# Optimization experiments

Measured on AMD Instinct MI355X. Metric: run time of the kernel, lower is better.

Reference implementation:

```python
import jax, jax.numpy as jnp
import numpy as np

ALPHABET = 8
DIM = 128
SEQ_LEN = 8192
POWER_ITERS = 200


def setup_inputs() -> dict:
    key = jax.random.key(0)
    k1, k2, k3 = jax.random.split(key, 3)
    return {
        "Kraus_op_re": jax.random.uniform(k1, (ALPHABET, DIM, DIM), dtype=jnp.float32),
        "Kraus_op_im": jax.random.uniform(k2, (ALPHABET, DIM, DIM), dtype=jnp.float32),
        "sequence": jax.random.randint(k3, (SEQ_LEN,), 0, ALPHABET),
    }


def _leading_eig(K):
    # K: [A, d, d] complex. Power iteration on the transfer map and its adjoint.
    d = K.shape[-1]
    Kc = K.conj()

    def body_r(rhor, _):
        # rhov = sum_x K_x @ rhor @ K_x^H
        rhov = jnp.einsum("aij,jk,alk->il", K, rhor, Kc)
        mu = jnp.trace(rhov).real
        return rhov / mu.astype(rhov.dtype), None

    rhor, _ = jax.lax.scan(body_r, jnp.eye(d, dtype=K.dtype) / d, None, length=POWER_ITERS)

    def body_l(carry, _):
        rhol, _ = carry
        # rhov = sum_x K_x^H @ rhol @ K_x
        rhov = jnp.einsum("aji,jk,akl->il", Kc, rhol, K)
        mu = jnp.trace(rhov).real
        return (rhov / mu.astype(rhov.dtype), mu), None

    (rhol, mu), _ = jax.lax.scan(
        body_l, (jnp.eye(d, dtype=K.dtype), jnp.asarray(1.0, jnp.float32)), None, length=POWER_ITERS
    )
    return rhor, rhol, mu


def reference(Kraus_op_re, Kraus_op_im, sequence):
    K = Kraus_op_re.astype(jnp.complex64) + 1j * Kraus_op_im.astype(jnp.complex64)
    rhor, rhol, lam = _leading_eig(K)
    # normalize so that trace(rho @ rhol) == 1
    rho0 = rhor / jnp.trace(rhor @ rhol).real.astype(rhor.dtype)
    Kn = K / jnp.sqrt(lam).astype(K.dtype)  # Kraus ops rescaled by sqrt(leading eigenvalue)
    L = sequence.shape[0]

    def step(carry, inp):
        rho, logp = carry
        i, x = inp
        Kx = Kn[x]
        rho = Kx @ rho @ Kx.conj().T
        px = jnp.where(i == L - 1, jnp.trace(rho @ rhol).real, jnp.trace(rho).real)
        logp = logp - jnp.log2(px)
        rho = rho / px.astype(rho.dtype)
        return (rho, logp), None

    (_, log_p), _ = jax.lax.scan(
        step, (rho0, jnp.asarray(0.0, jnp.float32)), (jnp.arange(L), sequence)
    )
    return log_p[None]  # matches torch.tensor([0.0]) accumulator shape (1,)
```

## Files before the change

kernel.cpp:

```cpp
#include <hip/hip_runtime.h>

typedef unsigned int u32;
typedef unsigned short u16;
typedef __attribute__((ext_vector_type(4))) float f32x4;
typedef __attribute__((ext_vector_type(8))) short s16x8;
typedef __attribute__((ext_vector_type(4))) u32 u32x4;

#define DIMN 128
#define MATN (DIMN*DIMN)
#define NA 8
#define LSEQ 8192
#define NTOK (LSEQ/2)
#define PITERS 4
#define S1SH 5
#define S2SH 6
#define CHSH 7
#define P2SH 8
#define GCH 256
#define GLG 16

struct WS {
  float2 *Kc;
  u16 *Kb, *P2b, *rho, *nodes0, *nodes1, *rootR, *rootI;
  int *tok, *E0, *E1, *Eroot;
  float *trbuf;
  float *out;
};

__device__ __forceinline__ u16 f2bf(float x){
  u32 u = __float_as_uint(x);
  u32 r = (u + 0x7FFFu + ((u >> 16) & 1u)) >> 16;
  return (u16)r;
}
__device__ __forceinline__ float bf2f(u16 u){ return __uint_as_float(((u32)u) << 16); }
__device__ __forceinline__ u32 cvtpk(float lo, float hi){
  u32 r; asm("v_cvt_pk_bf16_f32 %0, %1, %2" : "=v"(r) : "v"(lo), "v"(hi)); return r;
}
__device__ __forceinline__ s16x8 negi(s16x8 v){
  return __builtin_bit_cast(s16x8, __builtin_bit_cast(u32x4, v) ^ 0x80008000u);
}
__device__ __forceinline__ int swz16(int maj, int b){
  return maj*256 + (((((b >> 4) + maj*5) & 15) << 4) | (b & 15));
}
__device__ __forceinline__ void cfma2(float2& c, float2 a, float2 b){
  c.x = fmaf(a.x, b.x, c.x); c.x = fmaf(-a.y, b.y, c.x);
  c.y = fmaf(a.x, b.y, c.y); c.y = fmaf(a.y, b.x, c.y);
}
template<int CA, int CB>
__device__ __forceinline__ void cmfma(s16x8 a_r, s16x8 a_i, s16x8 b_r, s16x8 b_i,
                                      f32x4& qr, f32x4& qi){
  s16x8 t1 = (CA ^ CB) ? a_i : negi(a_i);
  s16x8 t2 = CB ? negi(a_r) : a_r;
  s16x8 t3 = CA ? negi(a_i) : a_i;
  qr = __builtin_amdgcn_mfma_f32_16x16x32_bf16(a_r, b_r, qr, 0,0,0);
  qr = __builtin_amdgcn_mfma_f32_16x16x32_bf16(t1,  b_i, qr, 0,0,0);
  qi = __builtin_amdgcn_mfma_f32_16x16x32_bf16(t2,  b_i, qi, 0,0,0);
  qi = __builtin_amdgcn_mfma_f32_16x16x32_bf16(t3,  b_r, qi, 0,0,0);
}

__global__ __launch_bounds__(256) void k_init(const float* Kre, const float* Kim,
                                              const int* seq, WS w){
  int gid = blockIdx.x*256 + threadIdx.x;
  int gsz = gridDim.x*256;
  for (int i = gid; i < NA*MATN; i += gsz){
    int x = i / MATN, rem = i - x*MATN, r = rem >> 7, c = rem & 127;
    float re = Kre[i], im = Kim[i];
    w.Kc[i] = make_float2(re, im);
    u16* b = w.Kb + (size_t)x*4*MATN;
    b[rem] = f2bf(re); b[MATN + rem] = f2bf(im);
    b[2*MATN + c*128 + r] = f2bf(re); b[3*MATN + c*128 + r] = f2bf(im);
  }
  for (int i = gid; i < NTOK; i += gsz)
    w.tok[i] = seq[2*i+1]*NA + seq[2*i];
  for (int i = gid; i < 4*MATN; i += gsz){
    int plane = (i >> 14) & 1, rem = i & (MATN-1);
    u16 v = (plane == 0 && (rem >> 7) == (rem & 127)) ? f2bf(1.f) : (u16)0;
    w.rho[i] = v;
  }
  if (gid < 32) w.trbuf[gid] = 0.f;
}

__global__ __launch_bounds__(256) void k_p2(WS w){
  __shared__ float2 As[16][33], Bs[16][33];
  int blk = blockIdx.x, mat = blk >> 4, tile = blk & 15;
  int a = mat >> 3, b = mat & 7;
  int row0 = (tile>>2)*32, col0 = (tile&3)*32;
  int t = threadIdx.x, ti = t & 15, tk = t >> 4;
  const float2* A = w.Kc + a*MATN;
  const float2* B = w.Kc + b*MATN;
  float2 acc[4] = {{0,0},{0,0},{0,0},{0,0}};
  for (int k0 = 0; k0 < 128; k0 += 16){
    { int r = t >> 4, kk = t & 15;
      As[kk][r]    = A[(row0+r)*DIMN + k0+kk];
      As[kk][r+16] = A[(row0+r+16)*DIMN + k0+kk]; }
    { int kk = t >> 5, c = t & 31;
      Bs[kk][c]   = B[(k0+kk)*DIMN + col0+c];
      Bs[kk+8][c] = B[(k0+kk+8)*DIMN + col0+c]; }
    __syncthreads();
    #pragma unroll
    for (int jj = 0; jj < 16; jj++){
      float2 a0 = As[jj][ti], a1 = As[jj][ti+16];
      float2 b0 = Bs[jj][tk], b1 = Bs[jj][tk+16];
      cfma2(acc[0], a0, b0); cfma2(acc[1], a0, b1);
      cfma2(acc[2], a1, b0); cfma2(acc[3], a1, b1);
    }
    __syncthreads();
  }
  const float sc = 1.f/(1<<P2SH);
  u16* base = w.P2b + (size_t)mat*4*MATN;
  int rr[4] = {row0+ti, row0+ti, row0+ti+16, row0+ti+16};
  int cc[4] = {col0+tk, col0+tk+16, col0+tk, col0+tk+16};
  #pragma unroll
  for (int i = 0; i < 4; i++){
    u16 vr = f2bf(acc[i].x*sc), vi = f2bf(acc[i].y*sc);
    base[rr[i]*128 + cc[i]] = vr;            base[MATN + rr[i]*128 + cc[i]] = vi;
    base[2*MATN + cc[i]*128 + rr[i]] = vr;   base[3*MATN + cc[i]*128 + rr[i]] = vi;
  }
}

__device__ __forceinline__ void loadA(const u16* Ar, const u16* Ai,
    int wr, int l15, int hi, s16x8 (&fr)[4][2], s16x8 (&fi)[4][2]){
  #pragma unroll
  for (int kk = 0; kk < 4; kk++){
    int kb = kk*32 + hi*8;
    #pragma unroll
    for (int m = 0; m < 2; m++){
      int r = wr + m*16 + l15;
      fr[kk][m] = *(const s16x8*)(Ar + r*128 + kb);
      fi[kk][m] = *(const s16x8*)(Ai + r*128 + kb);
    }
  }
}
__device__ __forceinline__ void ccomputeR(const s16x8 (&fr)[4][2], const s16x8 (&fi)[4][2],
    const char* Pr, const char* Pi, f32x4 (&qr)[2][4], f32x4 (&qi)[2][4],
    int wc, int l15, int hi){
  #pragma unroll
  for (int m=0;m<2;m++)
    #pragma unroll
    for (int n=0;n<4;n++){ qr[m][n] = (f32x4){0,0,0,0}; qi[m][n] = (f32x4){0,0,0,0}; }
  #pragma unroll
  for (int kk = 0; kk < 4; kk++){
    int kb = kk*32 + hi*8;
    #pragma unroll
    for (int n=0;n<4;n++){
      int c = wc + n*16 + l15;
      int o = swz16(c, kb*2);
      s16x8 b_r = *(const s16x8*)(Pr + o);
      s16x8 b_i = *(const s16x8*)(Pi + o);
      #pragma unroll
      for (int m=0;m<2;m++)
        cmfma<0,0>(fr[kk][m], fi[kk][m], b_r, b_i, qr[m][n], qi[m][n]);
    }
  }
}
__device__ __forceinline__ void pwrite8(char* Pr, char* Pi,
    f32x4 (&qr)[2][4], f32x4 (&qi)[2][4], float sc, int t){
  int wv = t>>6, lane = t&63, l15 = lane&15, hi = lane>>4;
  int wr = (wv>>1)*32, wc = (wv&1)*64;
  #pragma unroll
  for (int m=0;m<2;m++)
    #pragma unroll
    for (int n=0;n<4;n++){
      int c = wc + n*16 + l15, r0 = wr + m*16 + hi*4;
      uint2 pr, pi;
      pr.x = cvtpk(qr[m][n][0]*sc, qr[m][n][1]*sc);
      pr.y = cvtpk(qr[m][n][2]*sc, qr[m][n][3]*sc);
      pi.x = cvtpk(qi[m][n][0]*sc, qi[m][n][1]*sc);
      pi.y = cvtpk(qi[m][n][2]*sc, qi[m][n][3]*sc);
      int o = swz16(c, r0*2);
      *(uint2*)(Pr + o) = pr;
      *(uint2*)(Pi + o) = pi;
    }
}
__device__ __forceinline__ int renorm8(char* Pr, char* Pi,
    f32x4 (&qr)[2][4], f32x4 (&qi)[2][4], int t){
  int wv = t>>6, lane = t&63;
  float lm = 0.f;
  #pragma unroll
  for (int m=0;m<2;m++)
    #pragma unroll
    for (int n=0;n<4;n++)
      #pragma unroll
      for (int j=0;j<4;j++)
        lm = fmaxf(lm, fmaxf(fabsf(qr[m][n][j]), fabsf(qi[m][n][j])));
  #pragma unroll
  for (int o = 32; o > 0; o >>= 1) lm = fmaxf(lm, __shfl_xor(lm, o, 64));
  if (lane == 0) ((float*)Pr)[wv] = lm;
  __syncthreads();
  float mx = 0.f;
  #pragma unroll
  for (int i = 0; i < 8; i++) mx = fmaxf(mx, ((float*)Pr)[i]);
  int e = 0; if (mx > 0.f) frexpf(mx, &e);
  __syncthreads();
  pwrite8(Pr, Pi, qr, qi, ldexpf(1.f, -e), t);
  return e;
}
__device__ __forceinline__ void stage_cols(const u16* gr, const u16* gi,
                                           char* Pr, char* Pi, int t){
  #pragma unroll
  for (int i = 0; i < 4; i++){
    int chunk = t + i*512;
    int c = chunk >> 4, rr = chunk & 15;
    int o = swz16(c, rr*16);
    *(uint4*)(Pr + o) = *(const uint4*)(gr + c*128 + rr*8);
    *(uint4*)(Pi + o) = *(const uint4*)(gi + c*128 + rr*8);
  }
}
__device__ __forceinline__ void write_node(u16* dr, u16* di,
    const char* Pr, const char* Pi, bool rowLayout, int t){
  if (!rowLayout){
    #pragma unroll
    for (int i = 0; i < 4; i++){
      int chunk = t + i*512;
      int c = chunk >> 4, rr = chunk & 15;
      int o = swz16(c, rr*16);
      *(uint4*)(dr + c*128 + rr*8) = *(const uint4*)(Pr + o);
      *(uint4*)(di + c*128 + rr*8) = *(const uint4*)(Pi + o);
    }
  } else {
    for (int idx = t; idx < MATN; idx += 512){
      int r = idx >> 7, c = idx & 127;
      int o = swz16(c, r*2);
      dr[idx] = *(const u16*)(Pr + o);
      di[idx] = *(const u16*)(Pi + o);
    }
  }
}

__global__ __launch_bounds__(512,2) void k_chain(WS w){
  __shared__ __align__(16) char Pr[32768];
  __shared__ __align__(16) char Pi[32768];
  int p = blockIdx.x, t = threadIdx.x;
  int wv = t>>6, lane = t&63, l15 = lane&15, hi = lane>>4;
  int wr = (wv>>1)*32, wc = (wv&1)*64;
  int tok0 = w.tok[p*GLG];
  const u16* b0 = w.P2b + (size_t)tok0*4*MATN;
  stage_cols(b0 + 2*MATN, b0 + 3*MATN, Pr, Pi, t);
  s16x8 A1r[4][2], A1i[4][2], A2r[4][2], A2i[4][2];
  { const u16* tb = w.P2b + (size_t)w.tok[p*GLG + 1]*4*MATN;
    loadA(tb, tb + MATN, wr, l15, hi, A1r, A1i); }
  f32x4 qr[2][4], qi[2][4];
  int eLast = 0;
  __syncthreads();
  for (int s = 1; s < GLG; s += 2){
    if (s+1 < GLG){
      const u16* tb = w.P2b + (size_t)w.tok[p*GLG + s+1]*4*MATN;
      loadA(tb, tb + MATN, wr, l15, hi, A2r, A2i);
    }
    ccomputeR(A1r, A1i, Pr, Pi, qr, qi, wc, l15, hi);
    __syncthreads();
    if (s < GLG-1){ pwrite8(Pr, Pi, qr, qi, 1.f/(1<<CHSH), t); }
    else { eLast = renorm8(Pr, Pi, qr, qi, t); }
    __syncthreads();
    if (s+1 < GLG){
      if (s+2 < GLG){
        const u16* tb = w.P2b + (size_t)w.tok[p*GLG + s+2]*4*MATN;
        loadA(tb, tb + MATN, wr, l15, hi, A1r, A1i);
      }
      ccomputeR(A2r, A2i, Pr, Pi, qr, qi, wc, l15, hi);
      __syncthreads();
      if (s+1 < GLG-1){ pwrite8(Pr, Pi, qr, qi, 1.f/(1<<CHSH), t); }
      else { eLast = renorm8(Pr, Pi, qr, qi, t); }
      __syncthreads();
    }
  }
  u16* slot = w.nodes0 + (size_t)p*2*MATN;
  write_node(slot, slot + MATN, Pr, Pi, (p & 3) != 0, t);
  if (t == 0) w.E0[p] = P2SH*GLG + CHSH*(GLG-2) + eLast;
}

__global__ __launch_bounds__(512,2) void k_level(WS w, int lvl){
  __shared__ __align__(16) char Pr[32768];
  __shared__ __align__(16) char Pi[32768];
  int p = blockIdx.x, t = threadIdx.x;
  int wv = t>>6, lane = t&63, l15 = lane&15, hi = lane>>4;
  int wr = (wv>>1)*32, wc = (wv&1)*64;
  const u16* src = (lvl & 1) ? w.nodes0 : w.nodes1;
  u16* dst       = (lvl & 1) ? w.nodes1 : w.nodes0;
  const int* Es  = (lvl & 1) ? w.E0 : w.E1;
  int* Ed        = (lvl & 1) ? w.E1 : w.E0;
  const u16* B = src + (size_t)(4*p)*2*MATN;
  stage_cols(B, B + MATN, Pr, Pi, t);
  int E = Es[4*p] + Es[4*p+1] + Es[4*p+2] + Es[4*p+3];
  s16x8 A1r[4][2], A1i[4][2], A2r[4][2], A2i[4][2];
  { const u16* A = src + (size_t)(4*p+1)*2*MATN;
    loadA(A, A + MATN, wr, l15, hi, A1r, A1i); }
  f32x4 qr[2][4], qi[2][4];
  __syncthreads();
  { const u16* A = src + (size_t)(4*p+2)*2*MATN;
    loadA(A, A + MATN, wr, l15, hi, A2r, A2i); }
  ccomputeR(A1r, A1i, Pr, Pi, qr, qi, wc, l15, hi);
  __syncthreads();
  E += renorm8(Pr, Pi, qr, qi, t);
  __syncthreads();
  { const u16* A = src + (size_t)(4*p+3)*2*MATN;
    loadA(A, A + MATN, wr, l15, hi, A1r, A1i); }
  ccomputeR(A2r, A2i, Pr, Pi, qr, qi, wc, l15, hi);
  __syncthreads();
  E += renorm8(Pr, Pi, qr, qi, t);
  __syncthreads();
  ccomputeR(A1r, A1i, Pr, Pi, qr, qi, wc, l15, hi);
  __syncthreads();
  E += renorm8(Pr, Pi, qr, qi, t);
  __syncthreads();
  bool isRoot = (gridDim.x == 1);
  u16* slot = dst + (size_t)p*2*MATN;
  write_node(slot, slot + MATN, Pr, Pi, ((p & 3) != 0) || isRoot, t);
  if (t == 0) Ed[p] = E;
}

__global__ __launch_bounds__(512,1) void k_pow(WS w, int par){
  __shared__ __align__(16) char Rr[32768];
  __shared__ __align__(16) char Ri[32768];
  __shared__ __align__(16) char Yr[32768];
  __shared__ __align__(16) char Yi[32768];
  int b = blockIdx.x, side = b >> 3, rb = b & 7;
  int t = threadIdx.x, wv = t>>6, lane = t&63, l15 = lane&15, hi = lane>>4;
  const u16* rhoS = w.rho + (size_t)((par*2 + side)*2)*MATN;
  stage_cols(rhoS, rhoS + MATN, Rr, Ri, t);
  __syncthreads();
  {
    int x = wv;
    const u16* Ab = w.Kb + (size_t)(x*4 + (side ? 2 : 0))*MATN;
    const u16* Ar = Ab; const u16* Ai = Ab + MATN;
    f32x4 q1r[8], q1i[8];
    #pragma unroll
    for (int n=0;n<8;n++){ q1r[n] = (f32x4){0,0,0,0}; q1i[n] = (f32x4){0,0,0,0}; }
    #pragma unroll
    for (int kk = 0; kk < 4; kk++){
      int kb = kk*32 + hi*8;
      int r = rb*16 + l15;
      s16x8 a_r = *(const s16x8*)(Ar + r*128 + kb);
      s16x8 a_i = *(const s16x8*)(Ai + r*128 + kb);
      #pragma unroll
      for (int n=0;n<8;n++){
        int c = n*16 + l15;
        int o = swz16(c, kb*2);
        s16x8 b_r = *(const s16x8*)(Rr + o);
        s16x8 b_i = *(const s16x8*)(Ri + o);
        if (side == 0) cmfma<0,0>(a_r, a_i, b_r, b_i, q1r[n], q1i[n]);
        else           cmfma<1,0>(a_r, a_i, b_r, b_i, q1r[n], q1i[n]);
      }
    }
    const float sc = 1.f/(1<<S1SH);
    #pragma unroll
    for (int n=0;n<8;n++)
      #pragma unroll
      for (int q=0;q<4;q++){
        int lr = hi*4 + q, c = n*16 + l15;
        *(u16*)(Yr + x*4096 + swz16(lr, c*2)) = f2bf(q1r[n][q]*sc);
        *(u16*)(Yi + x*4096 + swz16(lr, c*2)) = f2bf(q1i[n][q]*sc);
      }
  }
  __syncthreads();
  {
    int c0 = wv*16, c = c0 + l15;
    f32x4 q2r = {0,0,0,0}, q2i = {0,0,0,0};
    #pragma unroll 2
    for (int x = 0; x < 8; x++){
      const u16* Bb = w.Kb + (size_t)(x*4 + (side ? 2 : 0))*MATN;
      const u16* Br = Bb; const u16* Bi = Bb + MATN;
      #pragma unroll
      for (int kk = 0; kk < 4; kk++){
        int kb = kk*32 + hi*8;
        s16x8 a_r = *(const s16x8*)(Yr + x*4096 + swz16(l15, kb*2));
        s16x8 a_i = *(const s16x8*)(Yi + x*4096 + swz16(l15, kb*2));
        s16x8 b_r = *(const s16x8*)(Br + c*128 + kb);
        s16x8 b_i = *(const s16x8*)(Bi + c*128 + kb);
        if (side == 0) cmfma<0,1>(a_r, a_i, b_r, b_i, q2r, q2i);
        else           cmfma<0,0>(a_r, a_i, b_r, b_i, q2r, q2i);
      }
    }
    const float sc = 1.f/(1<<S2SH);
    u16* Dr = w.rho + (size_t)(((par^1)*2 + side)*2)*MATN;
    u16* Di = Dr + MATN;
    int r0g = rb*16 + hi*4;
    uint2 pr, pi;
    pr.x = cvtpk(q2r[0]*sc, q2r[1]*sc); pr.y = cvtpk(q2r[2]*sc, q2r[3]*sc);
    pi.x = cvtpk(q2i[0]*sc, q2i[1]*sc); pi.y = cvtpk(q2i[2]*sc, q2i[3]*sc);
    *(uint2*)(Dr + c*128 + r0g) = pr;
    *(uint2*)(Di + c*128 + r0g) = pi;
    if (side == 1 && wv == rb){
      float tr = 0.f;
      #pragma unroll
      for (int q=0;q<4;q++) if (hi*4 + q == l15) tr += q2r[q]*sc;
      #pragma unroll
      for (int o = 32; o > 0; o >>= 1) tr += __shfl_xor(tr, o, 64);
      if (lane == 0) w.trbuf[par*16 + 8 + rb] = tr;
    }
  }
}

__global__ __launch_bounds__(512) void k_epi(WS w){
  __shared__ __align__(16) char T1r[32768];
  __shared__ __align__(16) char T1i[32768];
  int t = threadIdx.x, wv = t>>6, lane = t&63, l15 = lane&15, hi = lane>>4;
  int wr = (wv>>2)*64, wc = (wv&3)*32;
  f32x4 qr[4][2], qi[4][2];
  const u16* Ar = w.rho;
  const u16* Ai = Ar + MATN;
  #pragma unroll
  for (int m=0;m<4;m++)
    #pragma unroll
    for (int n=0;n<2;n++){ qr[m][n] = (f32x4){0,0,0,0}; qi[m][n] = (f32x4){0,0,0,0}; }
  #pragma unroll
  for (int kk = 0; kk < 4; kk++){
    int kb = kk*32 + hi*8;
    #pragma unroll
    for (int m=0;m<4;m++){
      int r = wr + m*16 + l15;
      s16x8 a_r = *(const s16x8*)(Ar + r*128 + kb);
      s16x8 a_i = *(const s16x8*)(Ai + r*128 + kb);
      #pragma unroll
      for (int n=0;n<2;n++){
        int c = wc + n*16 + l15;
        s16x8 b_r = *(const s16x8*)(w.rootR + c*128 + kb);
        s16x8 b_i = *(const s16x8*)(w.rootI + c*128 + kb);
        cmfma<0,0>(a_r, a_i, b_r, b_i, qr[m][n], qi[m][n]);
      }
    }
  }
  {
    const float sc = 1.f/(1<<CHSH);
    #pragma unroll
    for (int m=0;m<4;m++)
      #pragma unroll
      for (int n=0;n<2;n++){
        int c = wc + n*16 + l15, r0 = wr + m*16 + hi*4;
        uint2 pr, pi;
        pr.x = cvtpk(qr[m][n][0]*sc, qr[m][n][1]*sc);
        pr.y = cvtpk(qr[m][n][2]*sc, qr[m][n][3]*sc);
        pi.x = cvtpk(qi[m][n][0]*sc, qi[m][n][1]*sc);
        pi.y = cvtpk(qi[m][n][2]*sc, qi[m][n][3]*sc);
        int o = swz16(c, r0*2);
        *(uint2*)(T1r + o) = pr;
        *(uint2*)(T1i + o) = pi;
      }
  }
  __syncthreads();
  #pragma unroll
  for (int m=0;m<4;m++)
    #pragma unroll
    for (int n=0;n<2;n++){ qr[m][n] = (f32x4){0,0,0,0}; qi[m][n] = (f32x4){0,0,0,0}; }
  #pragma unroll
  for (int kk = 0; kk < 4; kk++){
    int kb = kk*32 + hi*8;
    #pragma unroll
    for (int m=0;m<4;m++){
      int r = wr + m*16 + l15;
      int o = swz16(r, kb*2);
      s16x8 a_r = *(const s16x8*)(T1r + o);
      s16x8 a_i = *(const s16x8*)(T1i + o);
      #pragma unroll
      for (int n=0;n<2;n++){
        int c = wc + n*16 + l15;
        s16x8 b_r = *(const s16x8*)(w.rootR + c*128 + kb);
        s16x8 b_i = *(const s16x8*)(w.rootI + c*128 + kb);
        cmfma<0,1>(a_r, a_i, b_r, b_i, qr[m][n], qi[m][n]);
      }
    }
  }
  __syncthreads();
  double* red = (double*)T1r;
  const u16* rlr = w.rho + (size_t)2*MATN;
  const u16* rli = rlr + MATN;
  double a1 = 0.0;
  #pragma unroll
  for (int m=0;m<4;m++)
    #pragma unroll
    for (int n=0;n<2;n++){
      int c = wc + n*16 + l15, r0 = wr + m*16 + hi*4;
      #pragma unroll
      for (int q=0;q<4;q++){
        int r = r0 + q;
        float lr = bf2f(rlr[r*128 + c]), li = bf2f(rli[r*128 + c]);
        a1 += (double)qr[m][n][q]*lr - (double)qi[m][n][q]*li;
      }
    }
  red[t] = a1; __syncthreads();
  for (int o = 256; o > 0; o >>= 1){ if (t < o) red[t] += red[t+o]; __syncthreads(); }
  double that = red[0]; __syncthreads();
  const u16* rrr = w.rho;
  const u16* rri = rrr + MATN;
  double a2 = 0.0;
  for (int idx = t; idx < MATN; idx += 512){
    int c = idx >> 7, r = idx & 127;
    float ar_ = bf2f(rrr[idx]), ai_ = bf2f(rri[idx]);
    float lr  = bf2f(rlr[r*128 + c]), li = bf2f(rli[r*128 + c]);
    a2 += (double)ar_*lr - (double)ai_*li;
  }
  red[t] = a2; __syncthreads();
  for (int o = 256; o > 0; o >>= 1){ if (t < o) red[t] += red[t+o]; __syncthreads(); }
  double trrl = red[0];
  if (t == 0){
    double T0 = 0.0, T1s = 0.0;
    for (int s = 0; s < 8; s++){ T0 += w.trbuf[8+s]; T1s += w.trbuf[16+8+s]; }
    double lam = ldexp(T1s / T0, S1SH + S2SH);
    double logp = (double)LSEQ * log2(lam) - 2.0*(double)w.Eroot[0] - (double)CHSH
                  - log2(fmax(that, 1e-300)) + log2(fmax(trrl, 1e-300));
    w.out[0] = (float)logp;
  }
}

static inline size_t aln256(size_t x){ return (x + 255) & ~(size_t)255; }

extern "C" void kernel_launch(void* const* d_in, const int* in_sizes, int n_in,
                              void* d_out, int out_size, void* d_ws, size_t ws_size,
                              hipStream_t stream){
  const float* Kre = (const float*)d_in[0];
  const float* Kim = (const float*)d_in[1];
  const int*   seq = (const int*)d_in[2];

  WS w{};
  char* p = (char*)d_ws;
  auto take = [&](size_t bytes)->char*{ char* r = p; p += aln256(bytes); return r; };
  w.Kc    = (float2*)take((size_t)NA*MATN*8);
  w.Kb    = (u16*)take((size_t)NA*4*MATN*2);
  w.P2b   = (u16*)take((size_t)64*4*MATN*2);
  w.rho   = (u16*)take((size_t)2*2*2*MATN*2);
  w.nodes0= (u16*)take((size_t)GCH*2*MATN*2);
  w.nodes1= (u16*)take((size_t)(GCH/4)*2*MATN*2);
  w.tok   = (int*)take(NTOK*4);
  w.E0    = (int*)take(GCH*4);
  w.E1    = (int*)take(GCH*4);
  w.trbuf = (float*)take(32*4);
  w.out = (float*)d_out;
  w.rootR = w.nodes0; w.rootI = w.nodes0 + MATN;
  w.Eroot = w.E0;

  hipLaunchKernelGGL(k_init, dim3(512), dim3(256), 0, stream, Kre, Kim, seq, w);
  hipLaunchKernelGGL(k_p2, dim3(64*16), dim3(256), 0, stream, w);
  hipLaunchKernelGGL(k_chain, dim3(GCH), dim3(512), 0, stream, w);
  for (int l = 1; l <= 4; l++)
    hipLaunchKernelGGL(k_level, dim3(GCH >> (2*l)), dim3(512), 0, stream, w, l);
  for (int k = 0; k < PITERS; k++)
    hipLaunchKernelGGL(k_pow, dim3(16), dim3(512), 0, stream, w, k & 1);
  hipLaunchKernelGGL(k_epi, dim3(1), dim3(512), 0, stream, w);
}
```

Baseline: 343.5 us.

## Widen chain reduction to 512 groups and add coalesced K bf16 conversion kernel

When the workspace is large enough, the sequence is split into 512 chain groups of 8 token-pairs instead of 256 groups of 16. This shortens the serial chain per block and fills more CUs, at the cost of one extra tree level with a radix-2 root. The K conversion moves into a tiled kernel that writes transposed bf16 copies through LDS, and k_p2 now reads raw float inputs and stages its transposed output through LDS for coalesced stores. The register double-buffered A-fragment prefetch in the chain and level kernels is dropped in favour of a simpler per-step load, which may expose global load latency.

```diff
diff --git a/kernel.cpp b/kernel.cpp
--- a/kernel.cpp
+++ b/kernel.cpp
@@ -16,15 +16,13 @@
 #define S2SH 6
 #define CHSH 7
 #define P2SH 8
-#define GCH 256
-#define GLG 16
 
 struct WS {
-  float2 *Kc;
   u16 *Kb, *P2b, *rho, *nodes0, *nodes1, *rootR, *rootI;
   int *tok, *E0, *E1, *Eroot;
   float *trbuf;
   float *out;
+  int G, g;
 };
 
 __device__ __forceinline__ u16 f2bf(float x){
@@ -58,18 +56,9 @@
   qi = __builtin_amdgcn_mfma_f32_16x16x32_bf16(t3,  b_r, qi, 0,0,0);
 }
 
-__global__ __launch_bounds__(256) void k_init(const float* Kre, const float* Kim,
-                                              const int* seq, WS w){
+__global__ __launch_bounds__(256) void k_init(const int* seq, WS w){
   int gid = blockIdx.x*256 + threadIdx.x;
   int gsz = gridDim.x*256;
-  for (int i = gid; i < NA*MATN; i += gsz){
-    int x = i / MATN, rem = i - x*MATN, r = rem >> 7, c = rem & 127;
-    float re = Kre[i], im = Kim[i];
-    w.Kc[i] = make_float2(re, im);
-    u16* b = w.Kb + (size_t)x*4*MATN;
-    b[rem] = f2bf(re); b[MATN + rem] = f2bf(im);
-    b[2*MATN + c*128 + r] = f2bf(re); b[3*MATN + c*128 + r] = f2bf(im);
-  }
   for (int i = gid; i < NTOK; i += gsz)
     w.tok[i] = seq[2*i+1]*NA + seq[2*i];
   for (int i = gid; i < 4*MATN; i += gsz){
@@ -80,22 +69,55 @@
   if (gid < 32) w.trbuf[gid] = 0.f;
 }
 
-__global__ __launch_bounds__(256) void k_p2(WS w){
+__global__ __launch_bounds__(256) void k_kb(const float* Kre, const float* Kim, WS w){
+  __shared__ u16 Lr[32][36], Li[32][36];
+  int blk = blockIdx.x, x = blk >> 4, tile = blk & 15;
+  int row0 = (tile>>2)*32, col0 = (tile&3)*32;
+  int t = threadIdx.x;
+  { int r = t>>3, cch = t&7;
+    size_t off = (size_t)x*MATN + (size_t)(row0+r)*128 + col0 + cch*4;
+    float4 vr = *(const float4*)(Kre + off);
+    float4 vi = *(const float4*)(Kim + off);
+    Lr[r][cch*4+0] = f2bf(vr.x); Lr[r][cch*4+1] = f2bf(vr.y);
+    Lr[r][cch*4+2] = f2bf(vr.z); Lr[r][cch*4+3] = f2bf(vr.w);
+    Li[r][cch*4+0] = f2bf(vi.x); Li[r][cch*4+1] = f2bf(vi.y);
+    Li[r][cch*4+2] = f2bf(vi.z); Li[r][cch*4+3] = f2bf(vi.w);
+  }
+  __syncthreads();
+  u16* b = w.Kb + (size_t)x*4*MATN;
+  { int r = t>>3, cch = t&7;
+    *(uint2*)&b[(row0+r)*128 + col0 + cch*4]        = *(uint2*)&Lr[r][cch*4];
+    *(uint2*)&b[MATN + (row0+r)*128 + col0 + cch*4] = *(uint2*)&Li[r][cch*4];
+  }
+  { int c = t>>3, rch = t&7;
+    ushort4 vr, vi;
+    vr.x = Lr[rch*4+0][c]; vr.y = Lr[rch*4+1][c];
+    vr.z = Lr[rch*4+2][c]; vr.w = Lr[rch*4+3][c];
+    vi.x = Li[rch*4+0][c]; vi.y = Li[rch*4+1][c];
+    vi.z = Li[rch*4+2][c]; vi.w = Li[rch*4+3][c];
+    *(ushort4*)&b[2*MATN + (col0+c)*128 + row0 + rch*4] = vr;
+    *(ushort4*)&b[3*MATN + (col0+c)*128 + row0 + rch*4] = vi;
+  }
+}
+
+__global__ __launch_bounds__(256) void k_p2(const float* Kre, const float* Kim, WS w){
   __shared__ float2 As[16][33], Bs[16][33];
   int blk = blockIdx.x, mat = blk >> 4, tile = blk & 15;
   int a = mat >> 3, b = mat & 7;
   int row0 = (tile>>2)*32, col0 = (tile&3)*32;
   int t = threadIdx.x, ti = t & 15, tk = t >> 4;
-  const float2* A = w.Kc + a*MATN;
-  const float2* B = w.Kc + b*MATN;
   float2 acc[4] = {{0,0},{0,0},{0,0},{0,0}};
   for (int k0 = 0; k0 < 128; k0 += 16){
     { int r = t >> 4, kk = t & 15;
-      As[kk][r]    = A[(row0+r)*DIMN + k0+kk];
-      As[kk][r+16] = A[(row0+r+16)*DIMN + k0+kk]; }
+      size_t i0 = (size_t)a*MATN + (size_t)(row0+r)*DIMN + k0+kk;
+      size_t i1 = i0 + 16*DIMN;
+      As[kk][r]    = make_float2(Kre[i0], Kim[i0]);
+      As[kk][r+16] = make_float2(Kre[i1], Kim[i1]); }
     { int kk = t >> 5, c = t & 31;
-      Bs[kk][c]   = B[(k0+kk)*DIMN + col0+c];
-      Bs[kk+8][c] = B[(k0+kk+8)*DIMN + col0+c]; }
+      size_t i0 = (size_t)b*MATN + (size_t)(k0+kk)*DIMN + col0+c;
+      size_t i1 = i0 + 8*DIMN;
+      Bs[kk][c]   = make_float2(Kre[i0], Kim[i0]);
+      Bs[kk+8][c] = make_float2(Kre[i1], Kim[i1]); }
     __syncthreads();
     #pragma unroll
     for (int jj = 0; jj < 16; jj++){
@@ -106,41 +128,47 @@
     }
     __syncthreads();
   }
+  u16* Lr = (u16*)As; u16* Li = (u16*)Bs;
   const float sc = 1.f/(1<<P2SH);
+  Lr[ti*36+tk]         = f2bf(acc[0].x*sc); Li[ti*36+tk]         = f2bf(acc[0].y*sc);
+  Lr[ti*36+tk+16]      = f2bf(acc[1].x*sc); Li[ti*36+tk+16]      = f2bf(acc[1].y*sc);
+  Lr[(ti+16)*36+tk]    = f2bf(acc[2].x*sc); Li[(ti+16)*36+tk]    = f2bf(acc[2].y*sc);
+  Lr[(ti+16)*36+tk+16] = f2bf(acc[3].x*sc); Li[(ti+16)*36+tk+16] = f2bf(acc[3].y*sc);
+  __syncthreads();
   u16* base = w.P2b + (size_t)mat*4*MATN;
-  int rr[4] = {row0+ti, row0+ti, row0+ti+16, row0+ti+16};
-  int cc[4] = {col0+tk, col0+tk+16, col0+tk, col0+tk+16};
-  #pragma unroll
-  for (int i = 0; i < 4; i++){
-    u16 vr = f2bf(acc[i].x*sc), vi = f2bf(acc[i].y*sc);
-    base[rr[i]*128 + cc[i]] = vr;            base[MATN + rr[i]*128 + cc[i]] = vi;
-    base[2*MATN + cc[i]*128 + rr[i]] = vr;   base[3*MATN + cc[i]*128 + rr[i]] = vi;
-  }
-}
-
-__device__ __forceinline__ void loadA(const u16* Ar, const u16* Ai,
-    int wr, int l15, int hi, s16x8 (&fr)[4][2], s16x8 (&fi)[4][2]){
+  { int r = t>>3, cch = t&7;
+    *(uint2*)&base[(row0+r)*128 + col0 + cch*4]        = *(uint2*)&Lr[r*36 + cch*4];
+    *(uint2*)&base[MATN + (row0+r)*128 + col0 + cch*4] = *(uint2*)&Li[r*36 + cch*4];
+  }
+  { int c = t>>3, rch = t&7;
+    ushort4 vr, vi;
+    vr.x = Lr[(rch*4+0)*36 + c]; vr.y = Lr[(rch*4+1)*36 + c];
+    vr.z = Lr[(rch*4+2)*36 + c]; vr.w = Lr[(rch*4+3)*36 + c];
+    vi.x = Li[(rch*4+0)*36 + c]; vi.y = Li[(rch*4+1)*36 + c];
+    vi.z = Li[(rch*4+2)*36 + c]; vi.w = Li[(rch*4+3)*36 + c];
+    *(ushort4*)&base[2*MATN + (col0+c)*128 + row0 + rch*4] = vr;
+    *(ushort4*)&base[3*MATN + (col0+c)*128 + row0 + rch*4] = vi;
+  }
+}
+
+__device__ __forceinline__ void ccompute(const u16* Ar, const u16* Ai,
+    const char* Pr, const char* Pi, f32x4 (&qr)[2][4], f32x4 (&qi)[2][4], int t){
+  int wv = t>>6, lane = t&63, l15 = lane&15, hi = lane>>4;
+  int wr = (wv>>1)*32, wc = (wv&1)*64;
+  #pragma unroll
+  for (int m=0;m<2;m++)
+    #pragma unroll
+    for (int n=0;n<4;n++){ qr[m][n] = (f32x4){0,0,0,0}; qi[m][n] = (f32x4){0,0,0,0}; }
   #pragma unroll
   for (int kk = 0; kk < 4; kk++){
     int kb = kk*32 + hi*8;
-    #pragma unroll
-    for (int m = 0; m < 2; m++){
+    s16x8 a_r[2], a_i[2];
+    #pragma unroll
+    for (int m=0;m<2;m++){
       int r = wr + m*16 + l15;
-      fr[kk][m] = *(const s16x8*)(Ar + r*128 + kb);
-      fi[kk][m] = *(const s16x8*)(Ai + r*128 + kb);
-    }
-  }
-}
-__device__ __forceinline__ void ccomputeR(const s16x8 (&fr)[4][2], const s16x8 (&fi)[4][2],
-    const char* Pr, const char* Pi, f32x4 (&qr)[2][4], f32x4 (&qi)[2][4],
-    int wc, int l15, int hi){
-  #pragma unroll
-  for (int m=0;m<2;m++)
-    #pragma unroll
-    for (int n=0;n<4;n++){ qr[m][n] = (f32x4){0,0,0,0}; qi[m][n] = (f32x4){0,0,0,0}; }
-  #pragma unroll
-  for (int kk = 0; kk < 4; kk++){
-    int kb = kk*32 + hi*8;
+      a_r[m] = *(const s16x8*)(Ar + r*128 + kb);
+      a_i[m] = *(const s16x8*)(Ai + r*128 + kb);
+    }
     #pragma unroll
     for (int n=0;n<4;n++){
       int c = wc + n*16 + l15;
@@ -149,7 +177,7 @@
       s16x8 b_i = *(const s16x8*)(Pi + o);
       #pragma unroll
       for (int m=0;m<2;m++)
-        cmfma<0,0>(fr[kk][m], fi[kk][m], b_r, b_i, qr[m][n], qi[m][n]);
+        cmfma<0,0>(a_r[m], a_i[m], b_r, b_i, qr[m][n], qi[m][n]);
     }
   }
 }
@@ -231,81 +259,49 @@
   __shared__ __align__(16) char Pr[32768];
   __shared__ __align__(16) char Pi[32768];
   int p = blockIdx.x, t = threadIdx.x;
-  int wv = t>>6, lane = t&63, l15 = lane&15, hi = lane>>4;
-  int wr = (wv>>1)*32, wc = (wv&1)*64;
-  int tok0 = w.tok[p*GLG];
+  int tok0 = w.tok[p*w.g];
   const u16* b0 = w.P2b + (size_t)tok0*4*MATN;
   stage_cols(b0 + 2*MATN, b0 + 3*MATN, Pr, Pi, t);
-  s16x8 A1r[4][2], A1i[4][2], A2r[4][2], A2i[4][2];
-  { const u16* tb = w.P2b + (size_t)w.tok[p*GLG + 1]*4*MATN;
-    loadA(tb, tb + MATN, wr, l15, hi, A1r, A1i); }
   f32x4 qr[2][4], qi[2][4];
   int eLast = 0;
-  __syncthreads();
-  for (int s = 1; s < GLG; s += 2){
-    if (s+1 < GLG){
-      const u16* tb = w.P2b + (size_t)w.tok[p*GLG + s+1]*4*MATN;
-      loadA(tb, tb + MATN, wr, l15, hi, A2r, A2i);
-    }
-    ccomputeR(A1r, A1i, Pr, Pi, qr, qi, wc, l15, hi);
+  for (int s = 1; s < w.g; s++){
+    const u16* tb = w.P2b + (size_t)w.tok[p*w.g + s]*4*MATN;
     __syncthreads();
-    if (s < GLG-1){ pwrite8(Pr, Pi, qr, qi, 1.f/(1<<CHSH), t); }
-    else { eLast = renorm8(Pr, Pi, qr, qi, t); }
+    ccompute(tb, tb + MATN, Pr, Pi, qr, qi, t);
     __syncthreads();
-    if (s+1 < GLG){
-      if (s+2 < GLG){
-        const u16* tb = w.P2b + (size_t)w.tok[p*GLG + s+2]*4*MATN;
-        loadA(tb, tb + MATN, wr, l15, hi, A1r, A1i);
-      }
-      ccomputeR(A2r, A2i, Pr, Pi, qr, qi, wc, l15, hi);
-      __syncthreads();
-      if (s+1 < GLG-1){ pwrite8(Pr, Pi, qr, qi, 1.f/(1<<CHSH), t); }
-      else { eLast = renorm8(Pr, Pi, qr, qi, t); }
-      __syncthreads();
-    }
-  }
+    if (s < w.g-1) pwrite8(Pr, Pi, qr, qi, 1.f/(1<<CHSH), t);
+    else eLast = renorm8(Pr, Pi, qr, qi, t);
+  }
+  __syncthreads();
   u16* slot = w.nodes0 + (size_t)p*2*MATN;
   write_node(slot, slot + MATN, Pr, Pi, (p & 3) != 0, t);
-  if (t == 0) w.E0[p] = P2SH*GLG + CHSH*(GLG-2) + eLast;
-}
-
-__global__ __launch_bounds__(512,2) void k_level(WS w, int lvl){
+  if (t == 0) w.E0[p] = P2SH*w.g + CHSH*(w.g-2) + eLast;
+}
+
+__global__ __launch_bounds__(512,2) void k_level(WS w, int srcIs0, int radix,
+                                                 int mask, int isRoot){
   __shared__ __align__(16) char Pr[32768];
   __shared__ __align__(16) char Pi[32768];
   int p = blockIdx.x, t = threadIdx.x;
-  int wv = t>>6, lane = t&63, l15 = lane&15, hi = lane>>4;
-  int wr = (wv>>1)*32, wc = (wv&1)*64;
-  const u16* src = (lvl & 1) ? w.nodes0 : w.nodes1;
-  u16* dst       = (lvl & 1) ? w.nodes1 : w.nodes0;
-  const int* Es  = (lvl & 1) ? w.E0 : w.E1;
-  int* Ed        = (lvl & 1) ? w.E1 : w.E0;
-  const u16* B = src + (size_t)(4*p)*2*MATN;
+  const u16* src = srcIs0 ? w.nodes0 : w.nodes1;
+  u16* dst       = srcIs0 ? w.nodes1 : w.nodes0;
+  const int* Es  = srcIs0 ? w.E0 : w.E1;
+  int* Ed        = srcIs0 ? w.E1 : w.E0;
+  const u16* B = src + (size_t)(radix*p)*2*MATN;
   stage_cols(B, B + MATN, Pr, Pi, t);
-  int E = Es[4*p] + Es[4*p+1] + Es[4*p+2] + Es[4*p+3];
-  s16x8 A1r[4][2], A1i[4][2], A2r[4][2], A2i[4][2];
-  { const u16* A = src + (size_t)(4*p+1)*2*MATN;
-    loadA(A, A + MATN, wr, l15, hi, A1r, A1i); }
+  int E = 0;
+  for (int j = 0; j < radix; j++) E += Es[radix*p + j];
   f32x4 qr[2][4], qi[2][4];
-  __syncthreads();
-  { const u16* A = src + (size_t)(4*p+2)*2*MATN;
-    loadA(A, A + MATN, wr, l15, hi, A2r, A2i); }
-  ccomputeR(A1r, A1i, Pr, Pi, qr, qi, wc, l15, hi);
-  __syncthreads();
-  E += renorm8(Pr, Pi, qr, qi, t);
-  __syncthreads();
-  { const u16* A = src + (size_t)(4*p+3)*2*MATN;
-    loadA(A, A + MATN, wr, l15, hi, A1r, A1i); }
-  ccomputeR(A2r, A2i, Pr, Pi, qr, qi, wc, l15, hi);
-  __syncthreads();
-  E += renorm8(Pr, Pi, qr, qi, t);
-  __syncthreads();
-  ccomputeR(A1r, A1i, Pr, Pi, qr, qi, wc, l15, hi);
-  __syncthreads();
-  E += renorm8(Pr, Pi, qr, qi, t);
-  __syncthreads();
-  bool isRoot = (gridDim.x == 1);
+  for (int j = 1; j < radix; j++){
+    const u16* A = src + (size_t)(radix*p + j)*2*MATN;
+    __syncthreads();
+    ccompute(A, A + MATN, Pr, Pi, qr, qi, t);
+    __syncthreads();
+    E += renorm8(Pr, Pi, qr, qi, t);
+  }
+  __syncthreads();
   u16* slot = dst + (size_t)p*2*MATN;
-  write_node(slot, slot + MATN, Pr, Pi, ((p & 3) != 0) || isRoot, t);
+  write_node(slot, slot + MATN, Pr, Pi, ((p & mask) != 0) || isRoot, t);
   if (t == 0) Ed[p] = E;
 }
 
@@ -511,28 +507,44 @@
   const float* Kim = (const float*)d_in[1];
   const int*   seq = (const int*)d_in[2];
 
+  size_t fixedBytes = aln256((size_t)NA*4*MATN*2) + aln256((size_t)64*4*MATN*2)
+                    + aln256((size_t)8*MATN*2) + aln256(NTOK*4)
+                    + 2*aln256(512*4) + aln256(32*4);
+  size_t need512 = fixedBytes + aln256((size_t)512*2*MATN*2) + aln256((size_t)128*2*MATN*2);
+  int G = (ws_size >= need512) ? 512 : 256;
+  int g = NTOK / G;
+
   WS w{};
   char* p = (char*)d_ws;
   auto take = [&](size_t bytes)->char*{ char* r = p; p += aln256(bytes); return r; };
-  w.Kc    = (float2*)take((size_t)NA*MATN*8);
   w.Kb    = (u16*)take((size_t)NA*4*MATN*2);
   w.P2b   = (u16*)take((size_t)64*4*MATN*2);
-  w.rho   = (u16*)take((size_t)2*2*2*MATN*2);
-  w.nodes0= (u16*)take((size_t)GCH*2*MATN*2);
-  w.nodes1= (u16*)take((size_t)(GCH/4)*2*MATN*2);
+  w.rho   = (u16*)take((size_t)8*MATN*2);
+  w.nodes0= (u16*)take((size_t)G*2*MATN*2);
+  w.nodes1= (u16*)take((size_t)(G/4)*2*MATN*2);
   w.tok   = (int*)take(NTOK*4);
-  w.E0    = (int*)take(GCH*4);
-  w.E1    = (int*)take(GCH*4);
+  w.E0    = (int*)take(512*4);
+  w.E1    = (int*)take(512*4);
   w.trbuf = (float*)take(32*4);
+  w.G = G; w.g = g;
   w.out = (float*)d_out;
-  w.rootR = w.nodes0; w.rootI = w.nodes0 + MATN;
-  w.Eroot = w.E0;
-
-  hipLaunchKernelGGL(k_init, dim3(512), dim3(256), 0, stream, Kre, Kim, seq, w);
-  hipLaunchKernelGGL(k_p2, dim3(64*16), dim3(256), 0, stream, w);
-  hipLaunchKernelGGL(k_chain, dim3(GCH), dim3(512), 0, stream, w);
-  for (int l = 1; l <= 4; l++)
-    hipLaunchKernelGGL(k_level, dim3(GCH >> (2*l)), dim3(512), 0, stream, w, l);
+
+  struct Lv { int blocks, srcIs0, radix, mask, isRoot; };
+  Lv lv512[5] = { {128,1,4,3,0},{32,0,4,3,0},{8,1,4,3,0},{2,0,4,1,0},{1,1,2,0,1} };
+  Lv lv256[4] = { {64,1,4,3,0},{16,0,4,3,0},{4,1,4,3,0},{1,0,4,0,1} };
+  Lv* lv = (G == 512) ? lv512 : lv256;
+  int nlv = (G == 512) ? 5 : 4;
+  if (lv[nlv-1].srcIs0){ w.rootR = w.nodes1; w.Eroot = w.E1; }
+  else                 { w.rootR = w.nodes0; w.Eroot = w.E0; }
+  w.rootI = w.rootR + MATN;
+
+  hipLaunchKernelGGL(k_init, dim3(64), dim3(256), 0, stream, seq, w);
+  hipLaunchKernelGGL(k_kb, dim3(NA*16), dim3(256), 0, stream, Kre, Kim, w);
+  hipLaunchKernelGGL(k_p2, dim3(64*16), dim3(256), 0, stream, Kre, Kim, w);
+  hipLaunchKernelGGL(k_chain, dim3(G), dim3(512), 0, stream, w);
+  for (int l = 0; l < nlv; l++)
+    hipLaunchKernelGGL(k_level, dim3(lv[l].blocks), dim3(512), 0, stream, w,
+                       lv[l].srcIs0, lv[l].radix, lv[l].mask, lv[l].isRoot);
   for (int k = 0; k < PITERS; k++)
     hipLaunchKernelGGL(k_pow, dim3(16), dim3(512), 0, stream, w, k & 1);
   hipLaunchKernelGGL(k_epi, dim3(1), dim3(512), 0, stream, w);
```

Result: faster. 328.3 us (-4.4%).
